# Kernel optimization log

Measured on AMD Instinct MI355X. Metric: run time of the kernel, lower is better.

Reference implementation:

```python
import jax, jax.numpy as jnp
import numpy as np

B, S, HID = 2, 2048, 4096
H, KV, D = 32, 8, 128
WINDOW = 512
ROPE_THETA = 10000.0


def _rope(x, positions):
    # x: [B, S, h, D]; neox rotate-half over full head_dim
    half = D // 2
    inv_freq = 1.0 / (ROPE_THETA ** (jnp.arange(0, half, dtype=jnp.float32) / half))
    ang = positions.astype(jnp.float32)[..., None] * inv_freq  # [B,S,half]
    cos = jnp.cos(ang)[:, :, None, :]
    sin = jnp.sin(ang)[:, :, None, :]
    x1, x2 = x[..., :half], x[..., half:]
    return jnp.concatenate([x1 * cos - x2 * sin, x2 * cos + x1 * sin], axis=-1)


def _smooth(x, filt):
    # x: [B, S, KV, D]; filt: [2, KV] -> out[t] = prev[t-1]*filt[0] + cur[t]*filt[1]
    prev = jnp.pad(x[:, :-1], ((0, 0), (1, 0), (0, 0), (0, 0)))  # zero at t=0
    return x * filt[1][None, None, :, None] + prev * filt[0][None, None, :, None]


def setup_inputs() -> dict:
    key = jax.random.key(0)
    k1, k2, k3, k4, k5 = jax.random.split(key, 5)
    return {
        "hidden_states": jax.random.normal(k1, (B, S, HID), jnp.float32) * 0.02,
        "positions": jnp.broadcast_to(jnp.arange(S, dtype=jnp.int32), (B, S)),
        "w_pack": jax.random.normal(k2, (HID, (H + 2 * KV) * D), jnp.float32) * (HID ** -0.5),
        "w_o": jax.random.normal(k3, (H * D, HID), jnp.float32) * ((H * D) ** -0.5),
        "conv_k": jax.random.normal(k4, (2, KV), jnp.float32) * 0.5,
        "conv_v": jax.random.normal(k5, (2, KV), jnp.float32) * 0.5,
    }


def reference(hidden_states, positions, w_pack, w_o, conv_k, conv_v):
    qkv = jnp.einsum("bsh,hf->bsf", hidden_states, w_pack)
    q = qkv[..., : H * D].reshape(B, S, H, D)
    k = qkv[..., H * D : (H + KV) * D].reshape(B, S, KV, D)
    v = qkv[..., (H + KV) * D :].reshape(B, S, KV, D)

    # causal depthwise smoothing of k/v (window 2), BEFORE rope
    k = _smooth(k, conv_k)
    v = _smooth(v, conv_v)

    q = _rope(q, positions)
    k = _rope(k, positions)

    g = H // KV  # GQA group size
    k_rep = jnp.repeat(k, g, axis=2)  # [B,S,H,D]
    v_rep = jnp.repeat(v, g, axis=2)

    scale = D ** -0.5
    scores = jnp.einsum("bqhd,bkhd->bhqk", q, k_rep) * scale
    qi = jnp.arange(S)[:, None]
    ki = jnp.arange(S)[None, :]
    mask = (ki <= qi) & (qi - ki < WINDOW)  # causal sliding window
    scores = jnp.where(mask[None, None], scores, jnp.float32(-1e30))
    probs = jax.nn.softmax(scores, axis=-1)
    attn = jnp.einsum("bhqk,bkhd->bqhd", probs, v_rep).reshape(B, S, H * D)
    return jnp.einsum("bsf,fh->bsh", attn, w_o)
```

## Files before the change

kernel.cpp:

```cpp
#include <hip/hip_runtime.h>
#include <stdint.h>

typedef unsigned short u16;
typedef unsigned int   u32;
typedef __bf16 bf16_t;
typedef __attribute__((ext_vector_type(8))) bf16_t bf16x8;
typedef __attribute__((ext_vector_type(4))) float   f32x4;

#define AS_GLOBAL __attribute__((address_space(1)))
#define AS_LDS    __attribute__((address_space(3)))

__device__ __forceinline__ void glds16(const u16* g, u16* l) {
  __builtin_amdgcn_global_load_lds((const AS_GLOBAL u32*)g, (AS_LDS u32*)l, 16, 0, 0);
}
__device__ __forceinline__ u16 f2bf(float f) {
  union { float f; u32 u; } a; a.f = f;
  return (u16)((a.u + 0x7FFFu + ((a.u >> 16) & 1u)) >> 16);
}
__device__ __forceinline__ float bf2f(u16 s) {
  union { u32 u; float f; } a; a.u = ((u32)s) << 16;
  return a.f;
}
union U16x8 { uint4 u; bf16x8 v; u16 h[8]; };

__global__ __launch_bounds__(256) void cvt_bf16(const float* __restrict__ X, u16* __restrict__ Y) {
  int i = blockIdx.x * 256 + threadIdx.x;
  float4 v = ((const float4*)X)[i];
  ushort4 o; o.x = f2bf(v.x); o.y = f2bf(v.y); o.z = f2bf(v.z); o.w = f2bf(v.w);
  ((ushort4*)Y)[i] = o;
}

__global__ __launch_bounds__(256) void cvt_transpose(const float* __restrict__ W, u16* __restrict__ Wt,
                                                     int K, int N) {
  __shared__ float t[64][65];
  const int n0 = blockIdx.x * 64, k0 = blockIdx.y * 64;
  const int tid = threadIdx.x;
  const int cr = tid >> 4, cc = (tid & 15) * 4;
#pragma unroll
  for (int p = 0; p < 4; ++p) {
    int r = p * 16 + cr;
    float4 v = *(const float4*)&W[(size_t)(k0 + r) * N + n0 + cc];
    t[r][cc] = v.x; t[r][cc + 1] = v.y; t[r][cc + 2] = v.z; t[r][cc + 3] = v.w;
  }
  __syncthreads();
#pragma unroll
  for (int p = 0; p < 4; ++p) {
    int rr = p * 16 + cr;
    ushort4 o;
    o.x = f2bf(t[cc + 0][rr]); o.y = f2bf(t[cc + 1][rr]);
    o.z = f2bf(t[cc + 2][rr]); o.w = f2bf(t[cc + 3][rr]);
    *(ushort4*)&Wt[(size_t)(n0 + rr) * K + k0 + cc] = o;
  }
}

__device__ __forceinline__ void stage256(const u16* gb, u16* ldst, int K, int kc, int tid, int w) {
#pragma unroll
  for (int s = 0; s < 2; ++s) {
    int t = s * 512 + tid;
    int row = t >> 2;
    int slot = (t & 3) ^ ((row >> 1) & 3);
    glds16(gb + (size_t)row * K + kc + slot * 8, ldst + s * 4096 + w * 512);
  }
}
template <int BN>
__device__ __forceinline__ void stageB(const u16* gb, u16* ldst, int K, int k0, int tid, int w) {
  constexpr int NB = BN / 64;
#pragma unroll
  for (int s = 0; s < NB; ++s) {
    int t = s * 512 + tid;
    int rr = t >> 2;
    int kh = rr >= BN ? 1 : 0;
    int row = rr - kh * BN;
    int slot = (t & 3) ^ ((row >> 1) & 3);
    glds16(gb + (size_t)row * K + k0 + kh * 32 + slot * 8, ldst + s * 4096 + w * 512);
  }
}

template <int BN, int WRITE_BF16>
__global__ __launch_bounds__(512, 2) void gemm8p(const u16* __restrict__ A, const u16* __restrict__ Bt,
                                                 void* __restrict__ C, int N, int K) {
  constexpr int NF = BN / 64;
  constexpr int A_U16 = 2 * 256 * 32;
  constexpr int B_U16 = 2 * BN * 32;
  constexpr int BUF = A_U16 + B_U16;
  __shared__ __align__(16) u16 lds[2 * BUF];

  const int tid = threadIdx.x;
  const int w = tid >> 6, l = tid & 63;
  const int col = l & 15, quad = l >> 4;
  const int m0 = blockIdx.y * 256, n0 = blockIdx.x * BN;
  const int wm = (w >> 2) * 128;
  const int wn = (w & 3) * (BN / 4);

  f32x4 acc[8][NF];
#pragma unroll
  for (int i = 0; i < 8; ++i)
#pragma unroll
    for (int j = 0; j < NF; ++j) acc[i][j] = f32x4{0.f, 0.f, 0.f, 0.f};

  const int sx = ((quad ^ ((col >> 1) & 3)) << 3);
  const int aoff = (wm + col) * 32 + sx;
  const int boff = (wn + col) * 32 + sx;

  const u16* Ab = A + (size_t)m0 * K;
  const u16* Bb = Bt + (size_t)n0 * K;
  const int NT = K >> 6;

  stage256(Ab, &lds[0], K, 0, tid, w);
  stageB<BN>(Bb, &lds[A_U16], K, 0, tid, w);
  stage256(Ab, &lds[8192], K, 32, tid, w);

  for (int t = 0; t < NT; ++t) {
    const int c = t & 1;
    const u16* lA = &lds[c * BUF];
    const u16* lB = &lds[c * BUF + A_U16];
    u16* nA = &lds[(c ^ 1) * BUF];
    u16* nB = &lds[(c ^ 1) * BUF + A_U16];
    const int kn = (t + 1) << 6;
    const bool last = (t == NT - 1);

    bf16x8 a[8], b[NF];
    asm volatile("s_waitcnt vmcnt(2)" ::: "memory");
    __builtin_amdgcn_s_barrier();
    __builtin_amdgcn_sched_barrier(0);
#pragma unroll
    for (int i = 0; i < 8; ++i) a[i] = *(const bf16x8*)&lA[i * 512 + aoff];
    b[0] = *(const bf16x8*)&lB[boff];
    b[1] = *(const bf16x8*)&lB[512 + boff];
    if (!last) stage256(Ab, nA, K, kn, tid, w);
    __builtin_amdgcn_s_setprio(1);
#pragma unroll
    for (int i = 0; i < 8; ++i) {
      acc[i][0] = __builtin_amdgcn_mfma_f32_16x16x32_bf16(a[i], b[0], acc[i][0], 0, 0, 0);
      acc[i][1] = __builtin_amdgcn_mfma_f32_16x16x32_bf16(a[i], b[1], acc[i][1], 0, 0, 0);
    }
    __builtin_amdgcn_s_setprio(0);
#pragma unroll
    for (int j = 2; j < NF; ++j) b[j] = *(const bf16x8*)&lB[j * 512 + boff];
    if (!last) stageB<BN>(Bb, nB, K, kn, tid, w);
    __builtin_amdgcn_s_setprio(1);
#pragma unroll
    for (int i = 0; i < 8; ++i)
#pragma unroll
      for (int j = 2; j < NF; ++j)
        acc[i][j] = __builtin_amdgcn_mfma_f32_16x16x32_bf16(a[i], b[j], acc[i][j], 0, 0, 0);
    __builtin_amdgcn_s_setprio(0);
    if (last) { asm volatile("s_waitcnt vmcnt(0)" ::: "memory"); }
    else if (BN == 256) { asm volatile("s_waitcnt vmcnt(6)" ::: "memory"); }
    else { asm volatile("s_waitcnt vmcnt(5)" ::: "memory"); }
    __builtin_amdgcn_s_barrier();
    __builtin_amdgcn_sched_barrier(0);
#pragma unroll
    for (int i = 0; i < 8; ++i) a[i] = *(const bf16x8*)&lA[8192 + i * 512 + aoff];
    b[0] = *(const bf16x8*)&lB[B_U16 / 2 + boff];
    b[1] = *(const bf16x8*)&lB[B_U16 / 2 + 512 + boff];
    if (!last) stage256(Ab, nA + 8192, K, kn + 32, tid, w);
    __builtin_amdgcn_s_setprio(1);
#pragma unroll
    for (int i = 0; i < 8; ++i) {
      acc[i][0] = __builtin_amdgcn_mfma_f32_16x16x32_bf16(a[i], b[0], acc[i][0], 0, 0, 0);
      acc[i][1] = __builtin_amdgcn_mfma_f32_16x16x32_bf16(a[i], b[1], acc[i][1], 0, 0, 0);
    }
    __builtin_amdgcn_s_setprio(0);
#pragma unroll
    for (int j = 2; j < NF; ++j) b[j] = *(const bf16x8*)&lB[B_U16 / 2 + j * 512 + boff];
    __builtin_amdgcn_s_setprio(1);
#pragma unroll
    for (int i = 0; i < 8; ++i)
#pragma unroll
      for (int j = 2; j < NF; ++j)
        acc[i][j] = __builtin_amdgcn_mfma_f32_16x16x32_bf16(a[i], b[j], acc[i][j], 0, 0, 0);
    __builtin_amdgcn_s_setprio(0);
  }

  if (WRITE_BF16) {
    u16* Cb = (u16*)C;
#pragma unroll
    for (int i = 0; i < 8; ++i)
#pragma unroll
      for (int r = 0; r < 4; ++r) {
        int m = m0 + wm + i * 16 + quad * 4 + r;
        u16* rp = Cb + (size_t)m * N + n0 + wn + col;
#pragma unroll
        for (int j = 0; j < NF; ++j) rp[j * 16] = f2bf(acc[i][j][r]);
      }
  } else {
    float* Cf = (float*)C;
#pragma unroll
    for (int i = 0; i < 8; ++i)
#pragma unroll
      for (int r = 0; r < 4; ++r) {
        int m = m0 + wm + i * 16 + quad * 4 + r;
        float* rp = Cf + (size_t)m * N + n0 + wn + col;
#pragma unroll
        for (int j = 0; j < NF; ++j) rp[j * 16] = acc[i][j][r];
      }
  }
}

__global__ __launch_bounds__(256) void smooth_rope(const u16* __restrict__ QKV, const int* __restrict__ pos,
                                                   const float* __restrict__ ck, const float* __restrict__ cv,
                                                   u16* __restrict__ Q, u16* __restrict__ Kk, u16* __restrict__ V) {
  const int s = blockIdx.x, b = blockIdx.y, tid = threadIdx.x;
  const size_t base = (size_t)(b * 2048 + s) * 6144;
  const bool hasPrev = (s > 0);
  const float p = (float)pos[b * 2048 + s];
  const float L2F = 0.20762050593046f;

  {
    const int h = tid >> 3, oc = tid & 7;
    U16x8 a, c;
    a.u = *(const uint4*)&QKV[base + h * 128 + oc * 8];
    c.u = *(const uint4*)&QKV[base + h * 128 + 64 + oc * 8];
    U16x8 o1, o2;
#pragma unroll
    for (int j = 0; j < 8; ++j) {
      int i = oc * 8 + j;
      float x1 = bf2f(a.h[j]), x2 = bf2f(c.h[j]);
      float ang = p * exp2f(-(float)i * L2F);
      float sn, cs; __sincosf(ang, &sn, &cs);
      o1.h[j] = f2bf(x1 * cs - x2 * sn);
      o2.h[j] = f2bf(x2 * cs + x1 * sn);
    }
    size_t o = ((size_t)(b * 32 + h) * 2048 + s) * 128 + oc * 8;
    *(uint4*)&Q[o] = o1.u;
    *(uint4*)&Q[o + 64] = o2.u;
  }
  if (tid < 64) {
    const int kv = tid >> 3, oc = tid & 7;
    const size_t off = base + 4096 + kv * 128 + oc * 8;
    const float f0 = ck[kv], f1 = ck[8 + kv];
    U16x8 a, c;
    a.u = *(const uint4*)&QKV[off];
    c.u = *(const uint4*)&QKV[off + 64];
    U16x8 pa, pc;
    pa.u = make_uint4(0, 0, 0, 0); pc.u = make_uint4(0, 0, 0, 0);
    if (hasPrev) {
      pa.u = *(const uint4*)&QKV[off - 6144];
      pc.u = *(const uint4*)&QKV[off - 6144 + 64];
    }
    U16x8 o1, o2;
#pragma unroll
    for (int j = 0; j < 8; ++j) {
      int i = oc * 8 + j;
      float x1 = bf2f(a.h[j]) * f1 + bf2f(pa.h[j]) * f0;
      float x2 = bf2f(c.h[j]) * f1 + bf2f(pc.h[j]) * f0;
      float ang = p * exp2f(-(float)i * L2F);
      float sn, cs; __sincosf(ang, &sn, &cs);
      o1.h[j] = f2bf(x1 * cs - x2 * sn);
      o2.h[j] = f2bf(x2 * cs + x1 * sn);
    }
    size_t o = ((size_t)(b * 8 + kv) * 2048 + s) * 128 + oc * 8;
    *(uint4*)&Kk[o] = o1.u;
    *(uint4*)&Kk[o + 64] = o2.u;
  } else if (tid < 192) {
    const int u2 = tid - 64;
    const int kv = u2 >> 4, oc = u2 & 15;
    const size_t off = base + 5120 + kv * 128 + oc * 8;
    const float f0 = cv[kv], f1 = cv[8 + kv];
    U16x8 a; a.u = *(const uint4*)&QKV[off];
    U16x8 pa; pa.u = make_uint4(0, 0, 0, 0);
    if (hasPrev) pa.u = *(const uint4*)&QKV[off - 6144];
    U16x8 o1;
#pragma unroll
    for (int j = 0; j < 8; ++j)
      o1.h[j] = f2bf(bf2f(a.h[j]) * f1 + bf2f(pa.h[j]) * f0);
    *(uint4*)&V[((size_t)(b * 8 + kv) * 2048 + s) * 128 + oc * 8] = o1.u;
  }
}

__global__ __launch_bounds__(256) void transpose_v(const u16* __restrict__ V, u16* __restrict__ Vt) {
  __shared__ u16 t[64][72];
  const int s0 = blockIdx.x * 64, d0 = blockIdx.y * 64, bkv = blockIdx.z;
  const u16* src = V + (size_t)bkv * 2048 * 128;
  u16* dst = Vt + (size_t)bkv * 128 * 2048;
  const int tid = threadIdx.x;
  for (int e = tid; e < 4096; e += 256) {
    int r = e >> 6, c = e & 63;
    t[r][c] = src[(size_t)(s0 + r) * 128 + d0 + c];
  }
  __syncthreads();
  for (int e = tid; e < 4096; e += 256) {
    int r = e >> 6, c = e & 63;
    dst[(size_t)(d0 + r) * 2048 + s0 + c] = t[c][r];
  }
}

__global__ __launch_bounds__(256) void attn_fwd(const u16* __restrict__ Q, const u16* __restrict__ Kk,
                                                const u16* __restrict__ Vt, u16* __restrict__ O) {
  __shared__ __align__(16) union {
    struct { u16 k[2][8192]; u16 v[2][8192]; u16 p[4][1152]; } s;
    u16 epi[64 * 136];
  } sm;
  const int tid = threadIdx.x, w = tid >> 6, l = tid & 63;
  const int col = l & 15, quad = l >> 4;
  const int orig = blockIdx.x + (blockIdx.y << 5);
  const int wid = (orig & 7) * 256 + (orig >> 3);
  const int q0 = (wid & 31) * 64;
  const int bh = wid >> 5;
  const int b = bh >> 5, h = bh & 31, kv = h >> 2;
  const int qrow = q0 + w * 16 + col;
  const int qlo = q0 + w * 16;

  bf16x8 qf[4];
  {
    const u16* qp = Q + ((size_t)((b * 32 + h) * 2048 + qrow)) * 128 + quad * 8;
#pragma unroll
    for (int dc = 0; dc < 4; ++dc) { U16x8 u; u.u = *(const uint4*)(qp + dc * 32); qf[dc] = u.v; }
  }
  const u16* Kbase = Kk + (size_t)(b * 8 + kv) * 2048 * 128;
  const u16* Vbase = Vt + (size_t)(b * 8 + kv) * 128 * 2048;

  f32x4 of[8];
#pragma unroll
  for (int i = 0; i < 8; ++i) of[i] = f32x4{0.f, 0.f, 0.f, 0.f};
  float m_i = -3.0e38f, l_i = 0.f;

  const int s_lo = q0 >= 511 ? q0 - 511 : 0;
  const int kt_lo = s_lo >> 6, kt_hi = q0 >> 6;

  auto issue = [&](int c, int k0) {
#pragma unroll
    for (int i = 0; i < 4; ++i) {
      const int base = (i * 4 + w) * 64;
      const int Lk = base + l;
      const int rk_ = Lk >> 4;
      const int sk_ = (Lk & 15) ^ (rk_ & 15);
      glds16(Kbase + (size_t)(k0 + rk_) * 128 + sk_ * 8, &sm.s.k[c][base * 8]);
      const int rv_ = Lk >> 3;
      const int sv_ = (Lk & 7) ^ (rv_ & 7);
      glds16(Vbase + (size_t)rv_ * 2048 + k0 + sv_ * 8, &sm.s.v[c][base * 8]);
    }
  };

  issue(0, kt_lo * 64);
  int cur = 0;

  for (int kt = kt_lo; kt <= kt_hi; ++kt) {
    const int k0 = kt * 64;
    if (kt < kt_hi) {
      issue(cur ^ 1, k0 + 64);
      asm volatile("s_waitcnt vmcnt(8)" ::: "memory");
    } else {
      asm volatile("s_waitcnt vmcnt(0)" ::: "memory");
    }
    __builtin_amdgcn_s_barrier();
    __builtin_amdgcn_sched_barrier(0);
    const u16* lK = sm.s.k[cur];
    const u16* lV = sm.s.v[cur];

    f32x4 st[4];
#pragma unroll
    for (int t = 0; t < 4; ++t) {
      st[t] = f32x4{0.f, 0.f, 0.f, 0.f};
#pragma unroll
      for (int dc = 0; dc < 4; ++dc) {
        bf16x8 a = *(const bf16x8*)&lK[(t * 16 + col) * 128 + (((dc * 4 + quad) ^ col) * 8)];
        st[t] = __builtin_amdgcn_mfma_f32_16x16x32_bf16(a, qf[dc], st[t], 0, 0, 0);
      }
    }
    const bool full = (k0 + 63 <= qlo) && (qlo + 15 - k0 < 512);
    float pmax = -3.0e38f;
#pragma unroll
    for (int t = 0; t < 4; ++t)
#pragma unroll
      for (int r = 0; r < 4; ++r) {
        float v = st[t][r] * 0.08838834764831845f;
        if (!full) {
          int key = k0 + t * 16 + quad * 4 + r;
          if (key > qrow || qrow - key >= 512) v = -1.0e30f;
        }
        st[t][r] = v;
        pmax = fmaxf(pmax, v);
      }
    pmax = fmaxf(pmax, __shfl_xor(pmax, 16, 64));
    pmax = fmaxf(pmax, __shfl_xor(pmax, 32, 64));
    float m_new = fmaxf(m_i, pmax);
    float alpha = __expf(m_i - m_new);
    float rsum = 0.f;
#pragma unroll
    for (int t = 0; t < 4; ++t) {
      u16 pk[4];
#pragma unroll
      for (int r = 0; r < 4; ++r) {
        float e = __expf(st[t][r] - m_new);
        rsum += e;
        pk[r] = f2bf(e);
      }
      u32 lo = (u32)pk[0] | ((u32)pk[1] << 16);
      u32 hi = (u32)pk[2] | ((u32)pk[3] << 16);
      *(uint2*)&sm.s.p[w][col * 72 + t * 16 + quad * 4] = make_uint2(lo, hi);
    }
    rsum += __shfl_xor(rsum, 16, 64);
    rsum += __shfl_xor(rsum, 32, 64);
    l_i = l_i * alpha + rsum;
    m_i = m_new;
#pragma unroll
    for (int i = 0; i < 8; ++i) {
      of[i][0] *= alpha; of[i][1] *= alpha; of[i][2] *= alpha; of[i][3] *= alpha;
    }
#pragma unroll
    for (int c = 0; c < 2; ++c) {
      bf16x8 pb = *(const bf16x8*)&sm.s.p[w][col * 72 + c * 32 + quad * 8];
#pragma unroll
      for (int dt = 0; dt < 8; ++dt) {
        bf16x8 a = *(const bf16x8*)&lV[(dt * 16 + col) * 64 + (((c * 4 + quad) ^ (col & 7)) * 8)];
        of[dt] = __builtin_amdgcn_mfma_f32_16x16x32_bf16(a, pb, of[dt], 0, 0, 0);
      }
    }
    __builtin_amdgcn_s_barrier();
    cur ^= 1;
  }
  float invl = 1.f / l_i;
  __syncthreads();
#pragma unroll
  for (int dt = 0; dt < 8; ++dt) {
    u16 pk[4];
#pragma unroll
    for (int r = 0; r < 4; ++r) pk[r] = f2bf(of[dt][r] * invl);
    u32 lo = (u32)pk[0] | ((u32)pk[1] << 16);
    u32 hi = (u32)pk[2] | ((u32)pk[3] << 16);
    *(uint2*)&sm.epi[(w * 16 + col) * 136 + dt * 16 + quad * 4] = make_uint2(lo, hi);
  }
  __syncthreads();
  for (int e = tid; e < 1024; e += 256) {
    int r = e >> 4, c = e & 15;
    uint4 v = *(const uint4*)&sm.epi[r * 136 + c * 8];
    *(uint4*)(O + ((size_t)(b * 2048 + q0 + r) * 4096 + h * 128 + c * 8)) = v;
  }
}

extern "C" void kernel_launch(void* const* d_in, const int* in_sizes, int n_in,
                              void* d_out, int out_size, void* d_ws, size_t ws_size,
                              hipStream_t stream) {
  const float* hs  = (const float*)d_in[0];
  const int*   pos = (const int*)d_in[1];
  const float* wp  = (const float*)d_in[2];
  const float* wo  = (const float*)d_in[3];
  const float* ck  = (const float*)d_in[4];
  const float* cv  = (const float*)d_in[5];
  float* out = (float*)d_out;
  char* ws = (char*)d_ws;

  u16* Xb   = (u16*)(ws);
  u16* Wt   = (u16*)(ws + 33554432);
  u16* QKV  = (u16*)(ws + 83886080);
  u16* Qb   = (u16*)(ws + 134217728);
  u16* Kb   = (u16*)(ws + 167772160);
  u16* Vb   = (u16*)(ws + 176160768);
  u16* Vtb  = (u16*)(ws + 184549376);
  u16* Attn = Xb;
  u16* Wot  = Wt;

  cvt_bf16<<<16384, 256, 0, stream>>>(hs, Xb);
  cvt_transpose<<<dim3(96, 64), 256, 0, stream>>>(wp, Wt, 4096, 6144);
  gemm8p<192, 1><<<dim3(32, 16), 512, 0, stream>>>(Xb, Wt, (void*)QKV, 6144, 4096);
  smooth_rope<<<dim3(2048, 2), 256, 0, stream>>>(QKV, pos, ck, cv, Qb, Kb, Vb);
  transpose_v<<<dim3(32, 2, 16), 256, 0, stream>>>(Vb, Vtb);
  attn_fwd<<<dim3(32, 64), 256, 0, stream>>>(Qb, Kb, Vtb, Attn);
  cvt_transpose<<<dim3(64, 64), 256, 0, stream>>>(wo, Wot, 4096, 4096);
  gemm8p<256, 0><<<dim3(16, 16), 512, 0, stream>>>(Attn, Wot, (void*)out, 4096, 4096);
}
```

Baseline: 652.7 us.

## Replace double-buffered GEMM with four-stage ring of 32-wide K slices

The projection GEMM's two-stage, 64-deep K pipeline with split A/B staging is replaced by a four-slot LDS ring. Each slot holds a 32-deep K slice of A and B, and loads are issued three slices ahead with graded vmcnt waits. The aim is to hide global-to-LDS latency better and to simplify scheduling into one barrier and one MFMA batch per step. In exchange, LDS use grows to 128KB per block, which likely prevents two blocks per CU. The BN=192 instantiation now stages 256 B rows, so it loads extra unused rows that run past the last tile into the adjacent workspace.

```diff
diff --git a/kernel.cpp b/kernel.cpp
--- a/kernel.cpp
+++ b/kernel.cpp
@@ -53,37 +53,13 @@
   }
 }
 
-__device__ __forceinline__ void stage256(const u16* gb, u16* ldst, int K, int kc, int tid, int w) {
-#pragma unroll
-  for (int s = 0; s < 2; ++s) {
-    int t = s * 512 + tid;
-    int row = t >> 2;
-    int slot = (t & 3) ^ ((row >> 1) & 3);
-    glds16(gb + (size_t)row * K + kc + slot * 8, ldst + s * 4096 + w * 512);
-  }
-}
-template <int BN>
-__device__ __forceinline__ void stageB(const u16* gb, u16* ldst, int K, int k0, int tid, int w) {
-  constexpr int NB = BN / 64;
-#pragma unroll
-  for (int s = 0; s < NB; ++s) {
-    int t = s * 512 + tid;
-    int rr = t >> 2;
-    int kh = rr >= BN ? 1 : 0;
-    int row = rr - kh * BN;
-    int slot = (t & 3) ^ ((row >> 1) & 3);
-    glds16(gb + (size_t)row * K + k0 + kh * 32 + slot * 8, ldst + s * 4096 + w * 512);
-  }
-}
+__device__ __forceinline__ bf16x8 mfma16(bf16x8 a, bf16x8 b, f32x4& acc);
 
 template <int BN, int WRITE_BF16>
-__global__ __launch_bounds__(512, 2) void gemm8p(const u16* __restrict__ A, const u16* __restrict__ Bt,
-                                                 void* __restrict__ C, int N, int K) {
+__global__ __launch_bounds__(512, 2) void gemm_dp(const u16* __restrict__ A, const u16* __restrict__ Bt,
+                                                  void* __restrict__ C, int N, int K) {
   constexpr int NF = BN / 64;
-  constexpr int A_U16 = 2 * 256 * 32;
-  constexpr int B_U16 = 2 * BN * 32;
-  constexpr int BUF = A_U16 + B_U16;
-  __shared__ __align__(16) u16 lds[2 * BUF];
+  __shared__ __align__(16) u16 lds[4 * 16384];
 
   const int tid = threadIdx.x;
   const int w = tid >> 6, l = tid & 63;
@@ -104,71 +80,45 @@
 
   const u16* Ab = A + (size_t)m0 * K;
   const u16* Bb = Bt + (size_t)n0 * K;
-  const int NT = K >> 6;
-
-  stage256(Ab, &lds[0], K, 0, tid, w);
-  stageB<BN>(Bb, &lds[A_U16], K, 0, tid, w);
-  stage256(Ab, &lds[8192], K, 32, tid, w);
+  const int NT = K >> 5;
+
+  auto issue = [&](int t) {
+    u16* dA = &lds[(t & 3) * 16384];
+    u16* dB = dA + 8192;
+    const int kc = t << 5;
+#pragma unroll
+    for (int s = 0; s < 2; ++s) {
+      int i = s * 512 + tid;
+      int row = i >> 2;
+      int slot = (i & 3) ^ ((row >> 1) & 3);
+      glds16(Ab + (size_t)row * K + kc + slot * 8, dA + s * 4096 + w * 512);
+      glds16(Bb + (size_t)row * K + kc + slot * 8, dB + s * 4096 + w * 512);
+    }
+  };
+
+  issue(0); issue(1); issue(2);
 
   for (int t = 0; t < NT; ++t) {
-    const int c = t & 1;
-    const u16* lA = &lds[c * BUF];
-    const u16* lB = &lds[c * BUF + A_U16];
-    u16* nA = &lds[(c ^ 1) * BUF];
-    u16* nB = &lds[(c ^ 1) * BUF + A_U16];
-    const int kn = (t + 1) << 6;
-    const bool last = (t == NT - 1);
-
-    bf16x8 a[8], b[NF];
-    asm volatile("s_waitcnt vmcnt(2)" ::: "memory");
+    const int rem = NT - 1 - t;
+    if (rem >= 2)      { asm volatile("s_waitcnt vmcnt(8)" ::: "memory"); }
+    else if (rem == 1) { asm volatile("s_waitcnt vmcnt(4)" ::: "memory"); }
+    else               { asm volatile("s_waitcnt vmcnt(0)" ::: "memory"); }
     __builtin_amdgcn_s_barrier();
     __builtin_amdgcn_sched_barrier(0);
-#pragma unroll
-    for (int i = 0; i < 8; ++i) a[i] = *(const bf16x8*)&lA[i * 512 + aoff];
-    b[0] = *(const bf16x8*)&lB[boff];
-    b[1] = *(const bf16x8*)&lB[512 + boff];
-    if (!last) stage256(Ab, nA, K, kn, tid, w);
+    if (t + 3 < NT) issue(t + 3);
+
+    const u16* dA = &lds[(t & 3) * 16384];
+    const u16* dB = dA + 8192;
+    bf16x8 a[8], b[NF];
+#pragma unroll
+    for (int i = 0; i < 8; ++i) a[i] = *(const bf16x8*)&dA[i * 512 + aoff];
+#pragma unroll
+    for (int j = 0; j < NF; ++j) b[j] = *(const bf16x8*)&dB[j * 512 + boff];
     __builtin_amdgcn_s_setprio(1);
 #pragma unroll
-    for (int i = 0; i < 8; ++i) {
-      acc[i][0] = __builtin_amdgcn_mfma_f32_16x16x32_bf16(a[i], b[0], acc[i][0], 0, 0, 0);
-      acc[i][1] = __builtin_amdgcn_mfma_f32_16x16x32_bf16(a[i], b[1], acc[i][1], 0, 0, 0);
-    }
-    __builtin_amdgcn_s_setprio(0);
-#pragma unroll
-    for (int j = 2; j < NF; ++j) b[j] = *(const bf16x8*)&lB[j * 512 + boff];
-    if (!last) stageB<BN>(Bb, nB, K, kn, tid, w);
-    __builtin_amdgcn_s_setprio(1);
-#pragma unroll
     for (int i = 0; i < 8; ++i)
 #pragma unroll
-      for (int j = 2; j < NF; ++j)
-        acc[i][j] = __builtin_amdgcn_mfma_f32_16x16x32_bf16(a[i], b[j], acc[i][j], 0, 0, 0);
-    __builtin_amdgcn_s_setprio(0);
-    if (last) { asm volatile("s_waitcnt vmcnt(0)" ::: "memory"); }
-    else if (BN == 256) { asm volatile("s_waitcnt vmcnt(6)" ::: "memory"); }
-    else { asm volatile("s_waitcnt vmcnt(5)" ::: "memory"); }
-    __builtin_amdgcn_s_barrier();
-    __builtin_amdgcn_sched_barrier(0);
-#pragma unroll
-    for (int i = 0; i < 8; ++i) a[i] = *(const bf16x8*)&lA[8192 + i * 512 + aoff];
-    b[0] = *(const bf16x8*)&lB[B_U16 / 2 + boff];
-    b[1] = *(const bf16x8*)&lB[B_U16 / 2 + 512 + boff];
-    if (!last) stage256(Ab, nA + 8192, K, kn + 32, tid, w);
-    __builtin_amdgcn_s_setprio(1);
-#pragma unroll
-    for (int i = 0; i < 8; ++i) {
-      acc[i][0] = __builtin_amdgcn_mfma_f32_16x16x32_bf16(a[i], b[0], acc[i][0], 0, 0, 0);
-      acc[i][1] = __builtin_amdgcn_mfma_f32_16x16x32_bf16(a[i], b[1], acc[i][1], 0, 0, 0);
-    }
-    __builtin_amdgcn_s_setprio(0);
-#pragma unroll
-    for (int j = 2; j < NF; ++j) b[j] = *(const bf16x8*)&lB[B_U16 / 2 + j * 512 + boff];
-    __builtin_amdgcn_s_setprio(1);
-#pragma unroll
-    for (int i = 0; i < 8; ++i)
-#pragma unroll
-      for (int j = 2; j < NF; ++j)
+      for (int j = 0; j < NF; ++j)
         acc[i][j] = __builtin_amdgcn_mfma_f32_16x16x32_bf16(a[i], b[j], acc[i][j], 0, 0, 0);
     __builtin_amdgcn_s_setprio(0);
   }
@@ -454,10 +404,10 @@
 
   cvt_bf16<<<16384, 256, 0, stream>>>(hs, Xb);
   cvt_transpose<<<dim3(96, 64), 256, 0, stream>>>(wp, Wt, 4096, 6144);
-  gemm8p<192, 1><<<dim3(32, 16), 512, 0, stream>>>(Xb, Wt, (void*)QKV, 6144, 4096);
+  gemm_dp<192, 1><<<dim3(32, 16), 512, 0, stream>>>(Xb, Wt, (void*)QKV, 6144, 4096);
   smooth_rope<<<dim3(2048, 2), 256, 0, stream>>>(QKV, pos, ck, cv, Qb, Kb, Vb);
   transpose_v<<<dim3(32, 2, 16), 256, 0, stream>>>(Vb, Vtb);
   attn_fwd<<<dim3(32, 64), 256, 0, stream>>>(Qb, Kb, Vtb, Attn);
   cvt_transpose<<<dim3(64, 64), 256, 0, stream>>>(wo, Wot, 4096, 4096);
-  gemm8p<256, 0><<<dim3(16, 16), 512, 0, stream>>>(Attn, Wot, (void*)out, 4096, 4096);
-}
+  gemm_dp<256, 0><<<dim3(16, 16), 512, 0, stream>>>(Attn, Wot, (void*)out, 4096, 4096);
+}
```

New measurement: 661.5 us. No clear change (+1.3%).
